# Kernel tuning notes

Measured on AMD Instinct MI355X. Metric: run time of the kernel, lower is better.

The kernel has to match this reference:

```python
import jax, jax.numpy as jnp
import numpy as np

STRIDE = 1
PADDING = 1
DILATION = 1


def setup_inputs() -> dict:
    key = jax.random.key(0)
    k1, k2 = jax.random.split(key)
    N, C_in, H, W = 32, 128, 56, 56
    C_out, ksz = 256, 3
    x = jax.random.normal(k1, (N, C_in, H, W), dtype=jnp.float32)
    # xavier_normal_ with gain sqrt(2): std = gain*sqrt(2/(fan_in+fan_out))
    fan_in = C_in * ksz * ksz
    fan_out = C_out * ksz * ksz
    std = np.sqrt(2.0) * np.sqrt(2.0 / (fan_in + fan_out))
    weight = jax.random.normal(k2, (C_out, C_in, ksz, ksz), dtype=jnp.float32) * jnp.float32(std)
    bias = jnp.zeros((C_out,), dtype=jnp.float32)
    return {"x": x, "weight": weight, "bias": bias}


def reference(x, weight, bias):
    # Faithful to conv2d(X, K, stride, padding, dilation, bias):
    # unfold (im2col) + matmul + fold is mathematically a standard cross-correlation
    # conv; expressed here with the efficient lax primitive.
    y = jax.lax.conv_general_dilated(
        x, weight,
        window_strides=(STRIDE, STRIDE),
        padding=[(PADDING, PADDING), (PADDING, PADDING)],
        rhs_dilation=(DILATION, DILATION),
        dimension_numbers=("NCHW", "OIHW", "NCHW"),
    )
    return y + bias[None, :, None, None]
```

## Files before the change

### kernel.cpp

```cpp
#include <hip/hip_runtime.h>
#include <hip/hip_bf16.h>


#define CIN   128
#define HH    56
#define WW    56
#define COUT  256
#define HW    3136
#define NIMG  32
#define NP    (NIMG * HW)
#define XPW   58
#define XPIX  (XPW * XPW)
#define XPAD_BYTES (NIMG * XPIX * CIN * 2)
#define WT_OFF     XPAD_BYTES

typedef __bf16 bf16x8 __attribute__((ext_vector_type(8)));
typedef float  f32x4  __attribute__((ext_vector_type(4)));

#define GLD16(g, l) __builtin_amdgcn_global_load_lds( \
    (const __attribute__((address_space(1))) void*)(g), \
    (__attribute__((address_space(3))) void*)(l), 16, 0, 0)

__device__ __forceinline__ unsigned pack_bf16(float a, float b) {
    return (__float_as_uint(b) & 0xFFFF0000u) | (__float_as_uint(a) >> 16);
}

__global__ __launch_bounds__(128) void prep_x(const float* __restrict__ x,
                                              __hip_bfloat16* __restrict__ xp) {
    __shared__ unsigned short t[HH * CIN];
    const int b  = blockIdx.x;
    const int n  = b / HH;
    const int y  = b - n * HH;
    const int ci = threadIdx.x;

    const float* src = x + ((size_t)(n * CIN + ci) * HW) + y * WW;
    #pragma unroll
    for (int j = 0; j < 14; ++j) {
        const float4 v = ((const float4*)src)[j];
        t[(4 * j + 0) * CIN + ci] = (unsigned short)(__float_as_uint(v.x) >> 16);
        t[(4 * j + 1) * CIN + ci] = (unsigned short)(__float_as_uint(v.y) >> 16);
        t[(4 * j + 2) * CIN + ci] = (unsigned short)(__float_as_uint(v.z) >> 16);
        t[(4 * j + 3) * CIN + ci] = (unsigned short)(__float_as_uint(v.w) >> 16);
    }

    const uint4 z = make_uint4(0, 0, 0, 0);
    if (ci < 32) {
        const int side = ci >> 4;
        const int j    = ci & 15;
        ((uint4*)(xp + ((size_t)n * XPIX + (y + 1) * XPW + side * 57) * CIN))[j] = z;
    }
    if (y == 0)
        for (int j = ci; j < 928; j += 128)
            ((uint4*)(xp + (size_t)n * XPIX * CIN))[j] = z;
    if (y == HH - 1)
        for (int j = ci; j < 928; j += 128)
            ((uint4*)(xp + ((size_t)n * XPIX + 57 * XPW) * CIN))[j] = z;

    __syncthreads();

    uint4* dst = (uint4*)(xp + ((size_t)n * XPIX + (y + 1) * XPW + 1) * CIN);
    const uint4* lsrc = (const uint4*)t;
    #pragma unroll
    for (int j = 0; j < 7; ++j)
        dst[j * 128 + ci] = lsrc[j * 128 + ci];
}

__global__ __launch_bounds__(256) void prep_w(const float* __restrict__ w,
                                              __hip_bfloat16* __restrict__ wt) {
    const int co = blockIdx.x * 2 + (threadIdx.x >> 7);
    const int ci = threadIdx.x & 127;
    const float* src = w + (size_t)(co * CIN + ci) * 9;
    #pragma unroll
    for (int tp = 0; tp < 9; ++tp)
        wt[(size_t)tp * (COUT * CIN) + co * CIN + ci] = __float2bfloat16(src[tp]);
}

__global__ __launch_bounds__(256) void conv_main(
    const char* __restrict__ xpb,
    const char* __restrict__ wtb,
    const float* __restrict__ bias,
    float* __restrict__ out)
{
    __shared__ __align__(16) char Alds[32768];
    __shared__ __align__(16) char Blds[32768];

    const int tid  = threadIdx.x;
    const int l    = tid & 63;
    const int wv   = tid >> 6;
    const int wm   = wv & 1;
    const int wn   = wv >> 1;
    const int l15  = l & 15;
    const int quad = l >> 4;

    const int idx = blockIdx.x;
    const int bm  = (idx >> 3) & 1;
    const int bn  = (idx >> 4) * 8 + (idx & 7);
    const int pbase  = bn * 128;
    const int cobase = bm * 128;

    unsigned aoff[8], boff[8];
    #pragma unroll
    for (int j = 0; j < 8; ++j) {
        const int c    = wv * 8 + j;
        const int row  = 4 * c + (l >> 4);
        const int gseg = (l & 15) ^ (row & 15);
        aoff[j] = (unsigned)((cobase + row) * 256 + gseg * 16);
        const int p   = pbase + row;
        const int n   = p / HW;
        const int rem = p - n * HW;
        const int y   = rem / WW;
        const int x   = rem - y * WW;
        boff[j] = (unsigned)((n * XPIX + y * XPW + x) * 256 + gseg * 16);
    }

    f32x4 acc[4][4];
    #pragma unroll
    for (int i = 0; i < 4; ++i)
        #pragma unroll
        for (int j = 0; j < 4; ++j)
            acc[i][j] = (f32x4){0.f, 0.f, 0.f, 0.f};

    #pragma unroll
    for (int t = 0; t < 9; ++t) {
        const int r = t / 3;
        const int s = t - 3 * r;
        const unsigned wo = (unsigned)(t * (COUT * CIN * 2));
        const unsigned bo = (unsigned)((r * XPW + s) * 256);

        __syncthreads();
        #pragma unroll
        for (int j = 0; j < 8; ++j) {
            const int c = wv * 8 + j;
            GLD16(wtb + wo + aoff[j], Alds + c * 1024);
            GLD16(xpb + bo + boff[j], Blds + c * 1024);
        }
        __syncthreads();

        #pragma unroll
        for (int kg = 0; kg < 4; ++kg) {
            bf16x8 af[4], bfr[4];
            #pragma unroll
            for (int mt = 0; mt < 4; ++mt) {
                const int row  = wm * 64 + mt * 16 + l15;
                const int segl = (kg * 4 + quad) ^ l15;
                af[mt] = *(const bf16x8*)(Alds + row * 256 + segl * 16);
            }
            #pragma unroll
            for (int nt = 0; nt < 4; ++nt) {
                const int row  = wn * 64 + nt * 16 + l15;
                const int segl = (kg * 4 + quad) ^ l15;
                bfr[nt] = *(const bf16x8*)(Blds + row * 256 + segl * 16);
            }
            #pragma unroll
            for (int mt = 0; mt < 4; ++mt)
                #pragma unroll
                for (int nt = 0; nt < 4; ++nt)
                    acc[mt][nt] = __builtin_amdgcn_mfma_f32_16x16x32_bf16(
                        af[mt], bfr[nt], acc[mt][nt], 0, 0, 0);
        }
    }

    #pragma unroll
    for (int nt = 0; nt < 4; ++nt) {
        const int pp = pbase + wn * 64 + nt * 16 + l15;
        const int n2 = pp / HW;
        const int r2 = pp - n2 * HW;
        float* ob = out + (size_t)n2 * (COUT * HW) + r2;
        #pragma unroll
        for (int mt = 0; mt < 4; ++mt) {
            const int co = cobase + wm * 64 + mt * 16 + quad * 4;
            const float4 bv = *(const float4*)(bias + co);
            f32x4 a = acc[mt][nt];
            ob[(size_t)(co + 0) * HW] = a[0] + bv.x;
            ob[(size_t)(co + 1) * HW] = a[1] + bv.y;
            ob[(size_t)(co + 2) * HW] = a[2] + bv.z;
            ob[(size_t)(co + 3) * HW] = a[3] + bv.w;
        }
    }
}

extern "C" void kernel_launch(void* const* d_in, const int* in_sizes, int n_in,
                              void* d_out, int out_size, void* d_ws, size_t ws_size,
                              hipStream_t stream) {
    const float* x = (const float*)d_in[0];
    const float* w = (const float*)d_in[1];
    const float* b = (const float*)d_in[2];
    char* ws = (char*)d_ws;
    __hip_bfloat16* xp = (__hip_bfloat16*)ws;
    __hip_bfloat16* wt = (__hip_bfloat16*)(ws + WT_OFF);

    prep_x<<<dim3(NIMG * HH), dim3(128), 0, stream>>>(x, xp);
    prep_w<<<dim3(128), dim3(256), 0, stream>>>(w, wt);
    conv_main<<<dim3((NP / 128) * 2), dim3(256), 0, stream>>>(
        (const char*)xp, (const char*)wt, b, (float*)d_out);
}
```

Baseline: 212.9 us.

## Fuse input transpose/bf16 conversion into conv kernel via per-row LDS slab

```diff
diff --git a/kernel.cpp b/kernel.cpp
--- a/kernel.cpp
+++ b/kernel.cpp
@@ -8,11 +8,10 @@
 #define COUT  256
 #define HW    3136
 #define NIMG  32
-#define NP    (NIMG * HW)
-#define XPW   58
-#define XPIX  (XPW * XPW)
-#define XPAD_BYTES (NIMG * XPIX * CIN * 2)
-#define WT_OFF     XPAD_BYTES
+#define SLABP 182
+#define SLAB_BYTES (SLABP * 256)
+#define ALDS_BYTES 32768
+#define WT_PLANE   (COUT * CIN * 2)
 
 typedef __bf16 bf16x8 __attribute__((ext_vector_type(8)));
 typedef float  f32x4  __attribute__((ext_vector_type(4)));
@@ -21,68 +20,23 @@
     (const __attribute__((address_space(1))) void*)(g), \
     (__attribute__((address_space(3))) void*)(l), 16, 0, 0)
 
-__device__ __forceinline__ unsigned pack_bf16(float a, float b) {
-    return (__float_as_uint(b) & 0xFFFF0000u) | (__float_as_uint(a) >> 16);
+__global__ __launch_bounds__(256) void prep_w(const float* __restrict__ w,
+                                              __hip_bfloat16* __restrict__ wt) {
+    const int L  = blockIdx.x * 256 + threadIdx.x;
+    const int ci = L & 127;
+    const int co = (L >> 7) & 255;
+    const int tp = L >> 15;
+    wt[L] = __float2bfloat16(w[(co * CIN + ci) * 9 + tp]);
 }
 
-__global__ __launch_bounds__(128) void prep_x(const float* __restrict__ x,
-                                              __hip_bfloat16* __restrict__ xp) {
-    __shared__ unsigned short t[HH * CIN];
-    const int b  = blockIdx.x;
-    const int n  = b / HH;
-    const int y  = b - n * HH;
-    const int ci = threadIdx.x;
-
-    const float* src = x + ((size_t)(n * CIN + ci) * HW) + y * WW;
-    #pragma unroll
-    for (int j = 0; j < 14; ++j) {
-        const float4 v = ((const float4*)src)[j];
-        t[(4 * j + 0) * CIN + ci] = (unsigned short)(__float_as_uint(v.x) >> 16);
-        t[(4 * j + 1) * CIN + ci] = (unsigned short)(__float_as_uint(v.y) >> 16);
-        t[(4 * j + 2) * CIN + ci] = (unsigned short)(__float_as_uint(v.z) >> 16);
-        t[(4 * j + 3) * CIN + ci] = (unsigned short)(__float_as_uint(v.w) >> 16);
-    }
-
-    const uint4 z = make_uint4(0, 0, 0, 0);
-    if (ci < 32) {
-        const int side = ci >> 4;
-        const int j    = ci & 15;
-        ((uint4*)(xp + ((size_t)n * XPIX + (y + 1) * XPW + side * 57) * CIN))[j] = z;
-    }
-    if (y == 0)
-        for (int j = ci; j < 928; j += 128)
-            ((uint4*)(xp + (size_t)n * XPIX * CIN))[j] = z;
-    if (y == HH - 1)
-        for (int j = ci; j < 928; j += 128)
-            ((uint4*)(xp + ((size_t)n * XPIX + 57 * XPW) * CIN))[j] = z;
-
-    __syncthreads();
-
-    uint4* dst = (uint4*)(xp + ((size_t)n * XPIX + (y + 1) * XPW + 1) * CIN);
-    const uint4* lsrc = (const uint4*)t;
-    #pragma unroll
-    for (int j = 0; j < 7; ++j)
-        dst[j * 128 + ci] = lsrc[j * 128 + ci];
-}
-
-__global__ __launch_bounds__(256) void prep_w(const float* __restrict__ w,
-                                              __hip_bfloat16* __restrict__ wt) {
-    const int co = blockIdx.x * 2 + (threadIdx.x >> 7);
-    const int ci = threadIdx.x & 127;
-    const float* src = w + (size_t)(co * CIN + ci) * 9;
-    #pragma unroll
-    for (int tp = 0; tp < 9; ++tp)
-        wt[(size_t)tp * (COUT * CIN) + co * CIN + ci] = __float2bfloat16(src[tp]);
-}
-
-__global__ __launch_bounds__(256) void conv_main(
-    const char* __restrict__ xpb,
-    const char* __restrict__ wtb,
+__global__ __launch_bounds__(256) void conv_fused(
+    const float* __restrict__ xin,
+    const char*  __restrict__ wtb,
     const float* __restrict__ bias,
     float* __restrict__ out)
 {
-    __shared__ __align__(16) char Alds[32768];
-    __shared__ __align__(16) char Blds[32768];
+    __shared__ __align__(16) char slab[SLAB_BYTES];
+    __shared__ __align__(16) char Alds[ALDS_BYTES];
 
     const int tid  = threadIdx.x;
     const int l    = tid & 63;
@@ -93,52 +47,74 @@
     const int quad = l >> 4;
 
     const int idx = blockIdx.x;
-    const int bm  = (idx >> 3) & 1;
-    const int bn  = (idx >> 4) * 8 + (idx & 7);
-    const int pbase  = bn * 128;
-    const int cobase = bm * 128;
+    const int cob = idx & 1;
+    const int n   = (idx >> 1) & 31;
+    const int y0  = idx >> 6;
+    const int cobase = cob * 128;
 
-    unsigned aoff[8], boff[8];
+    #pragma unroll
+    for (int i = 0; i < 12; ++i) {
+        const int z = tid + 256 * i;
+        if (z < SLAB_BYTES / 16) ((uint4*)slab)[z] = make_uint4(0, 0, 0, 0);
+    }
+
+    unsigned aoff[8];
     #pragma unroll
     for (int j = 0; j < 8; ++j) {
         const int c    = wv * 8 + j;
         const int row  = 4 * c + (l >> 4);
         const int gseg = (l & 15) ^ (row & 15);
         aoff[j] = (unsigned)((cobase + row) * 256 + gseg * 16);
-        const int p   = pbase + row;
-        const int n   = p / HW;
-        const int rem = p - n * HW;
-        const int y   = rem / WW;
-        const int x   = rem - y * WW;
-        boff[j] = (unsigned)((n * XPIX + y * XPW + x) * 256 + gseg * 16);
     }
 
-    f32x4 acc[4][4];
+    __syncthreads();
+
+    {
+        const int ci   = tid & 127;
+        const int half = tid >> 7;
+        const float* xplane = xin + (size_t)(n * CIN + ci) * HW;
+        #pragma unroll
+        for (int rr = 0; rr < 3; ++rr) {
+            const int gy = y0 - 1 + rr;
+            if (gy < 0 || gy >= HH) continue;
+            const float4* src = (const float4*)(xplane + gy * WW + half * 28);
+            #pragma unroll
+            for (int j = 0; j < 7; ++j) {
+                const float4 v = src[j];
+                const int P0 = rr * 58 + 1 + half * 28 + 4 * j;
+                const float vv[4] = {v.x, v.y, v.z, v.w};
+                #pragma unroll
+                for (int k = 0; k < 4; ++k) {
+                    const int P = P0 + k;
+                    const int a = P * 256 + ((((ci >> 3) ^ (P & 15)) << 4) | ((ci & 7) << 1));
+                    *(unsigned short*)(slab + a) = (unsigned short)(__float_as_uint(vv[k]) >> 16);
+                }
+            }
+        }
+    }
+
+    f32x4 acc[4][2];
     #pragma unroll
-    for (int i = 0; i < 4; ++i)
-        #pragma unroll
-        for (int j = 0; j < 4; ++j)
-            acc[i][j] = (f32x4){0.f, 0.f, 0.f, 0.f};
+    for (int i = 0; i < 4; ++i) {
+        acc[i][0] = (f32x4){0.f, 0.f, 0.f, 0.f};
+        acc[i][1] = (f32x4){0.f, 0.f, 0.f, 0.f};
+    }
 
     #pragma unroll
     for (int t = 0; t < 9; ++t) {
         const int r = t / 3;
         const int s = t - 3 * r;
-        const unsigned wo = (unsigned)(t * (COUT * CIN * 2));
-        const unsigned bo = (unsigned)((r * XPW + s) * 256);
+        const unsigned wo = (unsigned)(t * WT_PLANE);
 
         __syncthreads();
         #pragma unroll
-        for (int j = 0; j < 8; ++j) {
-            const int c = wv * 8 + j;
-            GLD16(wtb + wo + aoff[j], Alds + c * 1024);
-            GLD16(xpb + bo + boff[j], Blds + c * 1024);
-        }
+        for (int j = 0; j < 8; ++j)
+            GLD16(wtb + wo + aoff[j], Alds + (wv * 8 + j) * 1024);
         __syncthreads();
 
         #pragma unroll
         for (int kg = 0; kg < 4; ++kg) {
-            bf16x8 af[4], bfr[4];
+            bf16x8 af[4], bfr[2];
             #pragma unroll
             for (int mt = 0; mt < 4; ++mt) {
                 const int row  = wm * 64 + mt * 16 + l15;
@@ -146,35 +122,35 @@
                 af[mt] = *(const bf16x8*)(Alds + row * 256 + segl * 16);
             }
             #pragma unroll
-            for (int nt = 0; nt < 4; ++nt) {
-                const int row  = wn * 64 + nt * 16 + l15;
-                const int segl = (kg * 4 + quad) ^ l15;
-                bfr[nt] = *(const bf16x8*)(Blds + row * 256 + segl * 16);
+            for (int nt = 0; nt < 2; ++nt) {
+                const int pix  = r * 58 + wn * 32 + nt * 16 + l15 + s;
+                const int segl = (kg * 4 + quad) ^ (pix & 15);
+                bfr[nt] = *(const bf16x8*)(slab + pix * 256 + segl * 16);
             }
             #pragma unroll
             for (int mt = 0; mt < 4; ++mt)
                 #pragma unroll
-                for (int nt = 0; nt < 4; ++nt)
+                for (int nt = 0; nt < 2; ++nt)
                     acc[mt][nt] = __builtin_amdgcn_mfma_f32_16x16x32_bf16(
                         af[mt], bfr[nt], acc[mt][nt], 0, 0, 0);
         }
     }
 
+    float* obase = out + (size_t)n * (COUT * HW) + y0 * WW;
     #pragma unroll
-    for (int nt = 0; nt < 4; ++nt) {
-        const int pp = pbase + wn * 64 + nt * 16 + l15;
-        const int n2 = pp / HW;
-        const int r2 = pp - n2 * HW;
-        float* ob = out + (size_t)n2 * (COUT * HW) + r2;
-        #pragma unroll
-        for (int mt = 0; mt < 4; ++mt) {
-            const int co = cobase + wm * 64 + mt * 16 + quad * 4;
-            const float4 bv = *(const float4*)(bias + co);
-            f32x4 a = acc[mt][nt];
-            ob[(size_t)(co + 0) * HW] = a[0] + bv.x;
-            ob[(size_t)(co + 1) * HW] = a[1] + bv.y;
-            ob[(size_t)(co + 2) * HW] = a[2] + bv.z;
-            ob[(size_t)(co + 3) * HW] = a[3] + bv.w;
+    for (int nt = 0; nt < 2; ++nt) {
+        const int p = wn * 32 + nt * 16 + l15;
+        if (p < WW) {
+            #pragma unroll
+            for (int mt = 0; mt < 4; ++mt) {
+                const int co = cobase + wm * 64 + mt * 16 + quad * 4;
+                const float4 bv = *(const float4*)(bias + co);
+                f32x4 a = acc[mt][nt];
+                obase[(size_t)(co + 0) * HW + p] = a[0] + bv.x;
+                obase[(size_t)(co + 1) * HW + p] = a[1] + bv.y;
+                obase[(size_t)(co + 2) * HW + p] = a[2] + bv.z;
+                obase[(size_t)(co + 3) * HW + p] = a[3] + bv.w;
+            }
         }
     }
 }
@@ -185,12 +161,9 @@
     const float* x = (const float*)d_in[0];
     const float* w = (const float*)d_in[1];
     const float* b = (const float*)d_in[2];
-    char* ws = (char*)d_ws;
-    __hip_bfloat16* xp = (__hip_bfloat16*)ws;
-    __hip_bfloat16* wt = (__hip_bfloat16*)(ws + WT_OFF);
+    __hip_bfloat16* wt = (__hip_bfloat16*)d_ws;
 
-    prep_x<<<dim3(NIMG * HH), dim3(128), 0, stream>>>(x, xp);
-    prep_w<<<dim3(128), dim3(256), 0, stream>>>(w, wt);
-    conv_main<<<dim3((NP / 128) * 2), dim3(256), 0, stream>>>(
-        (const char*)xp, (const char*)wt, b, (float*)d_out);
+    prep_w<<<dim3(1152), dim3(256), 0, stream>>>(w, wt);
+    conv_fused<<<dim3(2 * NIMG * HH), dim3(256), 0, stream>>>(
+        x, (const char*)wt, b, (float*)d_out);
 }
```

Measured after the change: 234.2 us. 10.0% more time.
